# Performance work log

Hardware: AMD Instinct MI355X
Metric: run time of the kernel (lower is better)

The kernel has to match this reference:

```python
import math
import jax, jax.numpy as jnp
import numpy as np

B, N, F, FE = 16, 24, 128, 128   # crystals, atoms/crystal, atom feat, edge feat
NUM_Z = 100                       # num_atomic_numbers
GAUSS_STOP, BASIS_W = 6.0, 1.0
RADIUS_RATE = 1.0
N_CONV, N_FC, FC_F = 3, 4, 128
REP = 1                           # PBC replication per axis (27 images); exact for our cells
ZDIM = 2 * F + FE


def setup_inputs() -> dict:
    key = jax.random.key(0)
    ks = jax.random.split(key, 12)
    # cubic cells with side length in [8, 10) Angstrom -> rep per axis is exactly 1
    L = 8.0 + 2.0 * jax.random.uniform(ks[0], (B,))
    cell = L[:, None, None] * jnp.eye(3, dtype=jnp.float32)          # [B,3,3]
    frac = jax.random.uniform(ks[1], (B, N, 3))
    pos = jnp.einsum('bnd,bde->bne', frac, cell).reshape(B * N, 3)   # [B*N,3]
    atomic_numbers = jax.random.randint(ks[2], (B * N,), 1, NUM_Z + 1)
    batch = jnp.repeat(jnp.arange(B), N)
    emb = jax.random.normal(ks[3], (NUM_Z, F)) * 0.1                 # embedding table
    s = 1.0 / math.sqrt(ZDIM)
    conv_Wf = jax.random.normal(ks[4], (N_CONV, ZDIM, F)) * s
    conv_bf = jnp.zeros((N_CONV, F))
    conv_Ws = jax.random.normal(ks[5], (N_CONV, ZDIM, F)) * s
    conv_bs = jnp.zeros((N_CONV, F))
    sf = 1.0 / math.sqrt(FC_F)
    fc_W = jax.random.normal(ks[6], (N_FC - 1, FC_F, FC_F)) * sf
    fc_b = jnp.zeros((N_FC - 1, FC_F))
    W_out = jax.random.normal(ks[7], (FC_F, 1)) * sf
    b_out = jnp.zeros((1,))
    return {'pos': pos, 'cell': cell, 'emb': emb,
            'conv_Wf': conv_Wf, 'conv_bf': conv_bf,
            'conv_Ws': conv_Ws, 'conv_bs': conv_bs,
            'fc_W': fc_W, 'fc_b': fc_b, 'W_out': W_out, 'b_out': b_out,
            'atomic_numbers': atomic_numbers, 'batch': batch}


def _spectral_normalize(W, iters=5, eps=1e-12):
    # power iteration; sigma differentiable through W only (u,v detached) as in torch
    u = jnp.ones((W.shape[1],), W.dtype)
    u = u / jnp.linalg.norm(u)
    for _ in range(iters):
        v = W @ u
        v = v / (jnp.linalg.norm(v) + eps)
        u = W.T @ v
        u = u / (jnp.linalg.norm(u) + eps)
    u = jax.lax.stop_gradient(u)
    v = jax.lax.stop_gradient(v)
    sigma = v @ (W @ u)
    return W / sigma


def _forward(pos, cell, emb, conv_Wf, conv_bf, conv_Ws, conv_bs,
             fc_W, fc_b, W_out, b_out, atomic_numbers):
    # ---- graph construction (PBC all-pairs, fixed 27 images, masked) ----
    r = jnp.arange(-REP, REP + 1, dtype=cell.dtype)
    grid = jnp.stack(jnp.meshgrid(r, r, r, indexing='ij'), -1).reshape(-1, 3)  # [27,3]
    pbc = jnp.einsum('cd,bde->bce', grid, cell)                                # [B,27,3]
    posb = pos.reshape(B, N, 3)
    # disp[b,i,j,c] = pos_i - (pos_j + offset_c)
    disp = posb[:, :, None, None, :] - (posb[:, None, :, None, :] + pbc[:, None, None, :, :])
    dsqr = jnp.sum(disp * disp, -1)                                            # [B,N,N,27]
    cross = jnp.cross(cell[:, 1], cell[:, 2])
    vol = jnp.sum(cell[:, 0] * cross, -1)
    radius = RADIUS_RATE * (jnp.abs(vol) / N) ** (1.0 / 3.0)                   # [B]
    rb = radius[:, None, None, None]
    mask = (dsqr <= rb * rb) & (dsqr > 1e-4)
    dist = jnp.sqrt(jnp.maximum(dsqr, 1e-12))
    mf = mask.astype(pos.dtype)
    edge_w = (jnp.cos(dist * math.pi / rb) + 1.0) * mf                         # [B,N,N,27]
    # GaussianSmearing
    goff = jnp.linspace(0.0, GAUSS_STOP, FE)
    coeff = -0.5 / (BASIS_W * (goff[1] - goff[0])) ** 2
    edge_attr = jnp.exp(coeff * (dist[..., None] - goff) ** 2)                 # [B,N,N,27,FE]

    # ---- node features ----
    feat = jnp.tanh(emb[atomic_numbers - 1]).reshape(B, N, F)

    # ---- continuous graph convs (CGCNN-style gated conv, edge_weight scaled) ----
    for l in range(N_CONV):
        Wf, Ws = conv_Wf[l], conv_Ws[l]
        gi = feat @ Wf[:F]; gj = feat @ Wf[F:2 * F]
        ge = jnp.einsum('bijce,ef->bijcf', edge_attr, Wf[2 * F:])
        g = jax.nn.sigmoid(gi[:, :, None, None, :] + gj[:, None, :, None, :] + ge + conv_bf[l])
        si = feat @ Ws[:F]; sj = feat @ Ws[F:2 * F]
        se = jnp.einsum('bijce,ef->bijcf', edge_attr, Ws[2 * F:])
        sc = jax.nn.softplus(si[:, :, None, None, :] + sj[:, None, :, None, :] + se + conv_bs[l])
        msg = g * sc * edge_w[..., None]                                       # [B,N,N,27,F]
        feat = jax.nn.softplus(feat + msg.sum((2, 3)))                         # aggregate at i

    # ---- global mean pool + spectral-norm MLP head ----
    h = feat.mean(1)                                                           # [B,F]
    for l in range(N_FC - 1):
        h = jax.nn.softplus(h @ _spectral_normalize(fc_W[l]) + fc_b[l])
    return h @ W_out + b_out                                                   # [B,1]


def reference(pos, cell, emb, conv_Wf, conv_bf, conv_Ws, conv_bs,
              fc_W, fc_b, W_out, b_out, atomic_numbers, batch):
    return _forward(pos, cell, emb, conv_Wf, conv_bf, conv_Ws, conv_bs,
                    fc_W, fc_b, W_out, b_out, atomic_numbers)
```

## Files before the change

kernel.cpp:

```cpp
#include <hip/hip_runtime.h>
#include <math.h>

#define NB 16
#define NN 24
#define NA 384
#define FF 128
#define CC 27
#define MAXNBR 32

__device__ float g_sigma[4];
__device__ float g_projA[NA*4*FF];
__device__ float g_projB[NA*4*FF];
__device__ float g_feat [NA*FF];
__device__ __align__(128) int g_ctr[4*NB][32];
__device__ __align__(128) int g_sigdone[32];
__device__ __align__(128) int g_batchdone[32];

__device__ __forceinline__ float softplusf(float x){ return fmaxf(x,0.f) + log1pf(expf(-fabsf(x))); }
__device__ __forceinline__ float sigmoidf(float x){ return 1.f/(1.f+expf(-x)); }
__device__ __forceinline__ void st_agent(float* p, float v){
  __hip_atomic_store(p, v, __ATOMIC_RELAXED, __HIP_MEMORY_SCOPE_AGENT);
}
__device__ __forceinline__ float ld_agent(const float* p){
  return __hip_atomic_load(p, __ATOMIC_RELAXED, __HIP_MEMORY_SCOPE_AGENT);
}

__device__ __forceinline__ void band_dot(float dist, const float* __restrict__ Wf2,
                                         const float* __restrict__ Ws2, int f,
                                         float& ge, float& se)
{
  const float step  = 6.0f/127.0f;
  const float coeff = -0.5f/(step*step);
  int kmin = (int)ceilf(dist/step - 9.0f);
  kmin = kmin < 0 ? 0 : (kmin > 108 ? 108 : kmin);
  float g = 0.f, s = 0.f;
  #pragma unroll
  for (int t = 0; t < 20; t++) {
    int k = kmin + t;
    float dd = dist - step*(float)k;
    float a  = expf(coeff*dd*dd);
    g += a * Wf2[k*FF+f];
    s += a * Ws2[k*FF+f];
  }
  ge = g; se = s;
}

__device__ __forceinline__ float gemv_q(const float* __restrict__ Wf,
                                        const float* __restrict__ Ws,
                                        const float* s_ft, int q, int f)
{
  const float* W = (q==0) ? Wf : (q==1) ? (Wf + FF*FF) : (q==2) ? Ws : (Ws + FF*FF);
  float s = 0.f;
  #pragma unroll 16
  for (int k = 0; k < FF; k++) s += s_ft[k]*W[k*FF+f];
  return s;
}

__device__ __forceinline__ void publish(int* ctr)
{
  asm volatile("s_waitcnt vmcnt(0)" ::: "memory");
  __syncthreads();
  if (threadIdx.x == 0)
    __hip_atomic_fetch_add(ctr, 1, __ATOMIC_RELAXED, __HIP_MEMORY_SCOPE_AGENT);
}

__device__ __forceinline__ void wait_ge(int* ctr, int target)
{
  if (threadIdx.x == 0) {
    int guard = 0;
    while (__hip_atomic_load(ctr, __ATOMIC_RELAXED, __HIP_MEMORY_SCOPE_AGENT) < target) {
      __builtin_amdgcn_s_sleep(4);
      if (++guard > (1<<18)) break;
    }
  }
  __syncthreads();
}

__device__ __forceinline__ void edge_layer(int l, int q, int f, int n, int i,
       const float* __restrict__ projSrc,
       const float* __restrict__ conv_Wf, const float* __restrict__ conv_bf,
       const float* __restrict__ conv_Ws, const float* __restrict__ conv_bs,
       const int* s_nj, const float* s_nd, const float* s_nw,
       float (*s_p)[FF], float (*sm)[FF], float* s_ft)
{
  const float* Wf2 = conv_Wf + l*3*FF*FF + 2*FF*FF;
  const float* Ws2 = conv_Ws + l*3*FF*FF + 2*FF*FF;
  const float gi  = s_p[0][f];
  const float si  = s_p[2][f];
  const float bff = conv_bf[l*FF+f];
  const float bsf = conv_bs[l*FF+f];
  float msg = 0.f;
  for (int e = q; e < n; e += 4) {
    const int   jg   = s_nj[e];
    const float dist = s_nd[e];
    const float w    = s_nw[e];
    const float gj   = ld_agent(&projSrc[(jg*4+1)*FF+f]);
    const float sj   = ld_agent(&projSrc[(jg*4+3)*FF+f]);
    float ge, se;
    band_dot(dist, Wf2, Ws2, f, ge, se);
    msg += sigmoidf(gi + gj + ge + bff) * softplusf(si + sj + se + bsf) * w;
  }
  sm[q][f] = msg;
  __syncthreads();
  if (threadIdx.x < FF) {
    float v = softplusf(s_ft[f] + sm[0][f] + sm[1][f] + sm[2][f] + sm[3][f]);
    s_ft[f] = v;
  }
  __syncthreads();
}

__global__ void __launch_bounds__(512, 4)
k_fused(const float* __restrict__ pos, const float* __restrict__ cell,
        const float* __restrict__ emb,
        const float* __restrict__ conv_Wf, const float* __restrict__ conv_bf,
        const float* __restrict__ conv_Ws, const float* __restrict__ conv_bs,
        const float* __restrict__ fc_W,  const float* __restrict__ fc_b,
        const float* __restrict__ W_out, const float* __restrict__ b_out,
        const int* __restrict__ z, float* __restrict__ out)
{
  const int tid = threadIdx.x;
  const int q = tid >> 7, f = tid & 127;

  if (blockIdx.x < 3) {
    const int m = blockIdx.x;
    const float* W = fc_W + m*FF*FF;
    __shared__ float s_u[FF], s_v[FF], s_red2[FF];
    __shared__ float s_part2[4][FF];
    if (tid < FF) s_u[tid] = 0.08838834764831845f;
    __syncthreads();
    for (int it = 0; it < 5; it++) {
      { float p = 0.f;
        #pragma unroll
        for (int k = q*32; k < q*32+32; k++) p += W[f*FF+k]*s_u[k];
        s_part2[q][f] = p; }
      __syncthreads();
      if (tid < FF) { float s = s_part2[0][f]+s_part2[1][f]+s_part2[2][f]+s_part2[3][f];
                      s_v[f] = s; s_red2[f] = s*s; }
      __syncthreads();
      for (int st=64; st>0; st>>=1){ if (tid<st) s_red2[tid]+=s_red2[tid+st]; __syncthreads(); }
      float nv = sqrtf(s_red2[0]) + 1e-12f;
      __syncthreads();
      if (tid < FF) s_v[f] /= nv;
      __syncthreads();
      { float p = 0.f;
        #pragma unroll
        for (int r = q*32; r < q*32+32; r++) p += W[r*FF+f]*s_v[r];
        s_part2[q][f] = p; }
      __syncthreads();
      if (tid < FF) { float s = s_part2[0][f]+s_part2[1][f]+s_part2[2][f]+s_part2[3][f];
                      s_u[f] = s; s_red2[f] = s*s; }
      __syncthreads();
      for (int st=64; st>0; st>>=1){ if (tid<st) s_red2[tid]+=s_red2[tid+st]; __syncthreads(); }
      float nu = sqrtf(s_red2[0]) + 1e-12f;
      __syncthreads();
      if (tid < FF) s_u[f] /= nu;
      __syncthreads();
    }
    { float p = 0.f;
      #pragma unroll
      for (int k = q*32; k < q*32+32; k++) p += W[f*FF+k]*s_u[k];
      s_part2[q][f] = p; }
    __syncthreads();
    if (tid < FF) s_red2[f] = s_v[f]*(s_part2[0][f]+s_part2[1][f]+s_part2[2][f]+s_part2[3][f]);
    __syncthreads();
    for (int st=64; st>0; st>>=1){ if (tid<st) s_red2[tid]+=s_red2[tid+st]; __syncthreads(); }
    if (tid == 0) {
      st_agent(&g_sigma[m], s_red2[0]);
      asm volatile("s_waitcnt vmcnt(0)" ::: "memory");
      __hip_atomic_fetch_add(&g_sigdone[0], 1, __ATOMIC_RELAXED, __HIP_MEMORY_SCOPE_AGENT);
    }
    return;
  }

  const int i = (int)blockIdx.x - 3;
  const int b = i / NN;

  __shared__ float s_ft[FF];
  __shared__ float s_cell[9];
  __shared__ float s_rb;
  __shared__ int   s_cnt;
  __shared__ int   s_nj[MAXNBR];
  __shared__ float s_nd[MAXNBR];
  __shared__ float s_nw[MAXNBR];
  __shared__ float s_p[4][FF];
  __shared__ float sm[4][FF];
  __shared__ int   s_last;
  __shared__ float s_hh[FF], s_tmp[FF], s_red[FF];

  if (tid < FF) {
    int zi = z[i]; if (zi < 1) zi = 1; if (zi > 100) zi = 100;
    s_ft[tid] = tanhf(emb[(zi-1)*FF+tid]);
  }
  if (tid >= 256 && tid < 265) s_cell[tid-256] = cell[b*9 + tid - 256];
  if (tid == 500) s_cnt = 0;
  __syncthreads();
  if (tid == 0) {
    const float* c = s_cell;
    float cx = c[4]*c[8] - c[5]*c[7];
    float cy = c[5]*c[6] - c[3]*c[8];
    float cz = c[3]*c[7] - c[4]*c[6];
    float vol = c[0]*cx + c[1]*cy + c[2]*cz;
    s_rb = cbrtf(fabsf(vol)/(float)NN);
  }
  __syncthreads();
  {
    const float rb = s_rb, rb2 = rb*rb;
    const float pix = pos[i*3+0], piy = pos[i*3+1], piz = pos[i*3+2];
    const float PI = 3.14159265358979323846f;
    for (int cand = tid; cand < NN*CC; cand += 512) {
      int j = cand / CC, c = cand - j*CC;
      float gx = (float)(c/9) - 1.0f;
      float gy = (float)((c/3)%3) - 1.0f;
      float gz = (float)(c%3) - 1.0f;
      float ox = gx*s_cell[0] + gy*s_cell[3] + gz*s_cell[6];
      float oy = gx*s_cell[1] + gy*s_cell[4] + gz*s_cell[7];
      float oz = gx*s_cell[2] + gy*s_cell[5] + gz*s_cell[8];
      int jg = b*NN + j;
      float dx = pix - (pos[jg*3+0] + ox);
      float dy = piy - (pos[jg*3+1] + oy);
      float dz = piz - (pos[jg*3+2] + oz);
      float d2 = dx*dx + dy*dy + dz*dz;
      if (d2 <= rb2 && d2 > 1e-4f) {
        float dist = sqrtf(fmaxf(d2, 1e-4f));
        float w = cosf(dist*PI/rb) + 1.0f;
        int slot = atomicAdd(&s_cnt, 1);
        if (slot < MAXNBR) { s_nj[slot] = jg; s_nd[slot] = dist; s_nw[slot] = w; }
      }
    }
  }
  __syncthreads();
  const int n = (s_cnt > MAXNBR) ? MAXNBR : s_cnt;

  { float s0 = gemv_q(conv_Wf, conv_Ws, s_ft, q, f);
    s_p[q][f] = s0;
    st_agent(&g_projA[(i*4+q)*FF+f], s0); }
  publish(&g_ctr[0*NB+b][0]);
  wait_ge(&g_ctr[0*NB+b][0], NN);

  edge_layer(0, q, f, n, i, g_projA, conv_Wf, conv_bf, conv_Ws, conv_bs,
             s_nj, s_nd, s_nw, s_p, sm, s_ft);
  { float s1 = gemv_q(conv_Wf + 3*FF*FF, conv_Ws + 3*FF*FF, s_ft, q, f);
    s_p[q][f] = s1;
    st_agent(&g_projB[(i*4+q)*FF+f], s1); }
  publish(&g_ctr[1*NB+b][0]);
  wait_ge(&g_ctr[1*NB+b][0], NN);

  edge_layer(1, q, f, n, i, g_projB, conv_Wf, conv_bf, conv_Ws, conv_bs,
             s_nj, s_nd, s_nw, s_p, sm, s_ft);
  { float s2 = gemv_q(conv_Wf + 2*3*FF*FF, conv_Ws + 2*3*FF*FF, s_ft, q, f);
    s_p[q][f] = s2;
    st_agent(&g_projA[(i*4+q)*FF+f], s2); }
  publish(&g_ctr[2*NB+b][0]);
  wait_ge(&g_ctr[2*NB+b][0], NN);

  edge_layer(2, q, f, n, i, g_projA, conv_Wf, conv_bf, conv_Ws, conv_bs,
             s_nj, s_nd, s_nw, s_p, sm, s_ft);
  if (tid < FF) st_agent(&g_feat[i*FF+f], s_ft[f]);
  asm volatile("s_waitcnt vmcnt(0)" ::: "memory");
  __syncthreads();
  if (tid == 0)
    s_last = __hip_atomic_fetch_add(&g_ctr[3*NB+b][0], 1, __ATOMIC_RELAXED,
                                    __HIP_MEMORY_SCOPE_AGENT);
  __syncthreads();
  if (s_last != NN-1) return;

  if (tid == 0) {
    int guard = 0;
    while (__hip_atomic_load(&g_sigdone[0], __ATOMIC_RELAXED, __HIP_MEMORY_SCOPE_AGENT) < 3) {
      __builtin_amdgcn_s_sleep(4);
      if (++guard > (1<<18)) break;
    }
  }
  __syncthreads();
  if (tid < FF) {
    float s0 = 0.f;
    for (int a = 0; a < NN; a++) s0 += ld_agent(&g_feat[(b*NN+a)*FF+tid]);
    s_hh[tid] = s0/(float)NN;
  }
  __syncthreads();
  for (int l = 0; l < 3; l++) {
    { float p = 0.f;
      #pragma unroll
      for (int k = q*32; k < q*32+32; k++) p += s_hh[k]*fc_W[l*FF*FF + k*FF + f];
      sm[q][f] = p; }
    __syncthreads();
    if (tid < FF) {
      float s = sm[0][tid]+sm[1][tid]+sm[2][tid]+sm[3][tid];
      s_tmp[tid] = softplusf(s/ld_agent(&g_sigma[l]) + fc_b[l*FF+tid]);
    }
    __syncthreads();
    if (tid < FF) s_hh[tid] = s_tmp[tid];
    __syncthreads();
  }
  if (tid < FF) s_red[tid] = s_hh[tid]*W_out[tid];
  __syncthreads();
  if (tid < 64) {
    float t = s_red[tid] + s_red[tid+64];
    #pragma unroll
    for (int off = 32; off > 0; off >>= 1) t += __shfl_xor(t, off);
    if (tid == 0) {
      out[b] = t + b_out[0];
      __hip_atomic_store(&g_ctr[0*NB+b][0], 0, __ATOMIC_RELAXED, __HIP_MEMORY_SCOPE_AGENT);
      __hip_atomic_store(&g_ctr[1*NB+b][0], 0, __ATOMIC_RELAXED, __HIP_MEMORY_SCOPE_AGENT);
      __hip_atomic_store(&g_ctr[2*NB+b][0], 0, __ATOMIC_RELAXED, __HIP_MEMORY_SCOPE_AGENT);
      __hip_atomic_store(&g_ctr[3*NB+b][0], 0, __ATOMIC_RELAXED, __HIP_MEMORY_SCOPE_AGENT);
      int d = __hip_atomic_fetch_add(&g_batchdone[0], 1, __ATOMIC_RELAXED,
                                     __HIP_MEMORY_SCOPE_AGENT);
      if (d == NB-1) {
        __hip_atomic_store(&g_batchdone[0], 0, __ATOMIC_RELAXED, __HIP_MEMORY_SCOPE_AGENT);
        __hip_atomic_store(&g_sigdone[0],   0, __ATOMIC_RELAXED, __HIP_MEMORY_SCOPE_AGENT);
      }
    }
  }
}

extern "C" void kernel_launch(void* const* d_in, const int* in_sizes, int n_in,
                              void* d_out, int out_size, void* d_ws, size_t ws_size,
                              hipStream_t stream) {
  const float* pos     = (const float*)d_in[0];
  const float* cell    = (const float*)d_in[1];
  const float* emb     = (const float*)d_in[2];
  const float* conv_Wf = (const float*)d_in[3];
  const float* conv_bf = (const float*)d_in[4];
  const float* conv_Ws = (const float*)d_in[5];
  const float* conv_bs = (const float*)d_in[6];
  const float* fc_W    = (const float*)d_in[7];
  const float* fc_b    = (const float*)d_in[8];
  const float* W_out   = (const float*)d_in[9];
  const float* b_out   = (const float*)d_in[10];
  const int*   z       = (const int*)d_in[11];

  k_fused<<<NA+3, 512, 0, stream>>>(pos, cell, emb, conv_Wf, conv_bf,
                                    conv_Ws, conv_bs, fc_W, fc_b,
                                    W_out, b_out, z, (float*)d_out);
}
```

Baseline: 146.4 us.

## Process each crystal in one 1024-thread block with shared-memory projections

Replaces the per-atom grid of 384 blocks with one block per crystal. All 24 atoms' features, projections and neighbor lists now live in shared memory, which removes the global-memory projection buffers and the spin-wait counters between layers. The mean pool no longer needs a last-block election, and the pairwise neighbor search for the whole crystal runs inside the block. In exchange only 19 blocks occupy the GPU, so each block carries far more serial work per thread. The per-atom neighbor cap also drops from 32 to 24.

```diff
diff --git a/kernel.cpp b/kernel.cpp
--- a/kernel.cpp
+++ b/kernel.cpp
@@ -3,16 +3,12 @@
 
 #define NB 16
 #define NN 24
-#define NA 384
 #define FF 128
 #define CC 27
-#define MAXNBR 32
+#define MAXN 24
+#define NCAND (NN*NN*CC)
 
 __device__ float g_sigma[4];
-__device__ float g_projA[NA*4*FF];
-__device__ float g_projB[NA*4*FF];
-__device__ float g_feat [NA*FF];
-__device__ __align__(128) int g_ctr[4*NB][32];
 __device__ __align__(128) int g_sigdone[32];
 __device__ __align__(128) int g_batchdone[32];
 
@@ -45,71 +41,7 @@
   ge = g; se = s;
 }
 
-__device__ __forceinline__ float gemv_q(const float* __restrict__ Wf,
-                                        const float* __restrict__ Ws,
-                                        const float* s_ft, int q, int f)
-{
-  const float* W = (q==0) ? Wf : (q==1) ? (Wf + FF*FF) : (q==2) ? Ws : (Ws + FF*FF);
-  float s = 0.f;
-  #pragma unroll 16
-  for (int k = 0; k < FF; k++) s += s_ft[k]*W[k*FF+f];
-  return s;
-}
-
-__device__ __forceinline__ void publish(int* ctr)
-{
-  asm volatile("s_waitcnt vmcnt(0)" ::: "memory");
-  __syncthreads();
-  if (threadIdx.x == 0)
-    __hip_atomic_fetch_add(ctr, 1, __ATOMIC_RELAXED, __HIP_MEMORY_SCOPE_AGENT);
-}
-
-__device__ __forceinline__ void wait_ge(int* ctr, int target)
-{
-  if (threadIdx.x == 0) {
-    int guard = 0;
-    while (__hip_atomic_load(ctr, __ATOMIC_RELAXED, __HIP_MEMORY_SCOPE_AGENT) < target) {
-      __builtin_amdgcn_s_sleep(4);
-      if (++guard > (1<<18)) break;
-    }
-  }
-  __syncthreads();
-}
-
-__device__ __forceinline__ void edge_layer(int l, int q, int f, int n, int i,
-       const float* __restrict__ projSrc,
-       const float* __restrict__ conv_Wf, const float* __restrict__ conv_bf,
-       const float* __restrict__ conv_Ws, const float* __restrict__ conv_bs,
-       const int* s_nj, const float* s_nd, const float* s_nw,
-       float (*s_p)[FF], float (*sm)[FF], float* s_ft)
-{
-  const float* Wf2 = conv_Wf + l*3*FF*FF + 2*FF*FF;
-  const float* Ws2 = conv_Ws + l*3*FF*FF + 2*FF*FF;
-  const float gi  = s_p[0][f];
-  const float si  = s_p[2][f];
-  const float bff = conv_bf[l*FF+f];
-  const float bsf = conv_bs[l*FF+f];
-  float msg = 0.f;
-  for (int e = q; e < n; e += 4) {
-    const int   jg   = s_nj[e];
-    const float dist = s_nd[e];
-    const float w    = s_nw[e];
-    const float gj   = ld_agent(&projSrc[(jg*4+1)*FF+f]);
-    const float sj   = ld_agent(&projSrc[(jg*4+3)*FF+f]);
-    float ge, se;
-    band_dot(dist, Wf2, Ws2, f, ge, se);
-    msg += sigmoidf(gi + gj + ge + bff) * softplusf(si + sj + se + bsf) * w;
-  }
-  sm[q][f] = msg;
-  __syncthreads();
-  if (threadIdx.x < FF) {
-    float v = softplusf(s_ft[f] + sm[0][f] + sm[1][f] + sm[2][f] + sm[3][f]);
-    s_ft[f] = v;
-  }
-  __syncthreads();
-}
-
-__global__ void __launch_bounds__(512, 4)
+__global__ void __launch_bounds__(1024, 4)
 k_fused(const float* __restrict__ pos, const float* __restrict__ cell,
         const float* __restrict__ emb,
         const float* __restrict__ conv_Wf, const float* __restrict__ conv_bf,
@@ -119,80 +51,82 @@
         const int* __restrict__ z, float* __restrict__ out)
 {
   const int tid = threadIdx.x;
-  const int q = tid >> 7, f = tid & 127;
-
-  if (blockIdx.x < 3) {
-    const int m = blockIdx.x;
+
+  __shared__ float s_ft[NN*FF];
+  __shared__ float s_pj[NN*2*FF];
+  __shared__ float s_part2[4][FF];
+  __shared__ float s_hh[FF], s_tmp[FF], s_red[FF];
+  __shared__ float s_u[FF], s_v[FF];
+  __shared__ float s_pos[NN*3];
+  __shared__ float s_cell[9];
+  __shared__ float s_rb;
+  __shared__ int   s_cnt[NN];
+  __shared__ int   s_nbrj[NN*MAXN];
+  __shared__ float s_nbrd[NN*MAXN];
+  __shared__ float s_nbrw[NN*MAXN];
+
+  if (blockIdx.x >= NB) {
+    const int m = blockIdx.x - NB;
+    const int q = tid >> 7, f = tid & 127;
     const float* W = fc_W + m*FF*FF;
-    __shared__ float s_u[FF], s_v[FF], s_red2[FF];
-    __shared__ float s_part2[4][FF];
     if (tid < FF) s_u[tid] = 0.08838834764831845f;
     __syncthreads();
     for (int it = 0; it < 5; it++) {
-      { float p = 0.f;
+      if (tid < 512) { float p = 0.f;
         #pragma unroll
         for (int k = q*32; k < q*32+32; k++) p += W[f*FF+k]*s_u[k];
         s_part2[q][f] = p; }
       __syncthreads();
       if (tid < FF) { float s = s_part2[0][f]+s_part2[1][f]+s_part2[2][f]+s_part2[3][f];
-                      s_v[f] = s; s_red2[f] = s*s; }
-      __syncthreads();
-      for (int st=64; st>0; st>>=1){ if (tid<st) s_red2[tid]+=s_red2[tid+st]; __syncthreads(); }
-      float nv = sqrtf(s_red2[0]) + 1e-12f;
+                      s_v[f] = s; s_red[f] = s*s; }
+      __syncthreads();
+      for (int st=64; st>0; st>>=1){ if (tid<st) s_red[tid]+=s_red[tid+st]; __syncthreads(); }
+      float nv = sqrtf(s_red[0]) + 1e-12f;
       __syncthreads();
       if (tid < FF) s_v[f] /= nv;
       __syncthreads();
-      { float p = 0.f;
+      if (tid < 512) { float p = 0.f;
         #pragma unroll
         for (int r = q*32; r < q*32+32; r++) p += W[r*FF+f]*s_v[r];
         s_part2[q][f] = p; }
       __syncthreads();
       if (tid < FF) { float s = s_part2[0][f]+s_part2[1][f]+s_part2[2][f]+s_part2[3][f];
-                      s_u[f] = s; s_red2[f] = s*s; }
-      __syncthreads();
-      for (int st=64; st>0; st>>=1){ if (tid<st) s_red2[tid]+=s_red2[tid+st]; __syncthreads(); }
-      float nu = sqrtf(s_red2[0]) + 1e-12f;
+                      s_u[f] = s; s_red[f] = s*s; }
+      __syncthreads();
+      for (int st=64; st>0; st>>=1){ if (tid<st) s_red[tid]+=s_red[tid+st]; __syncthreads(); }
+      float nu = sqrtf(s_red[0]) + 1e-12f;
       __syncthreads();
       if (tid < FF) s_u[f] /= nu;
       __syncthreads();
     }
-    { float p = 0.f;
+    if (tid < 512) { float p = 0.f;
       #pragma unroll
       for (int k = q*32; k < q*32+32; k++) p += W[f*FF+k]*s_u[k];
       s_part2[q][f] = p; }
     __syncthreads();
-    if (tid < FF) s_red2[f] = s_v[f]*(s_part2[0][f]+s_part2[1][f]+s_part2[2][f]+s_part2[3][f]);
-    __syncthreads();
-    for (int st=64; st>0; st>>=1){ if (tid<st) s_red2[tid]+=s_red2[tid+st]; __syncthreads(); }
+    if (tid < FF) s_red[f] = s_v[f]*(s_part2[0][f]+s_part2[1][f]+s_part2[2][f]+s_part2[3][f]);
+    __syncthreads();
+    for (int st=64; st>0; st>>=1){ if (tid<st) s_red[tid]+=s_red[tid+st]; __syncthreads(); }
     if (tid == 0) {
-      st_agent(&g_sigma[m], s_red2[0]);
+      st_agent(&g_sigma[m], s_red[0]);
       asm volatile("s_waitcnt vmcnt(0)" ::: "memory");
       __hip_atomic_fetch_add(&g_sigdone[0], 1, __ATOMIC_RELAXED, __HIP_MEMORY_SCOPE_AGENT);
     }
     return;
   }
 
-  const int i = (int)blockIdx.x - 3;
-  const int b = i / NN;
-
-  __shared__ float s_ft[FF];
-  __shared__ float s_cell[9];
-  __shared__ float s_rb;
-  __shared__ int   s_cnt;
-  __shared__ int   s_nj[MAXNBR];
-  __shared__ float s_nd[MAXNBR];
-  __shared__ float s_nw[MAXNBR];
-  __shared__ float s_p[4][FF];
-  __shared__ float sm[4][FF];
-  __shared__ int   s_last;
-  __shared__ float s_hh[FF], s_tmp[FF], s_red[FF];
-
-  if (tid < FF) {
-    int zi = z[i]; if (zi < 1) zi = 1; if (zi > 100) zi = 100;
-    s_ft[tid] = tanhf(emb[(zi-1)*FF+tid]);
-  }
-  if (tid >= 256 && tid < 265) s_cell[tid-256] = cell[b*9 + tid - 256];
-  if (tid == 500) s_cnt = 0;
+  const int b = blockIdx.x;
+
+  if (tid < 9)    s_cell[tid] = cell[b*9 + tid];
+  if (tid < NN)   s_cnt[tid] = 0;
+  if (tid < NN*3) s_pos[tid] = pos[b*NN*3 + tid];
+  #pragma unroll
+  for (int it = 0; it < 3; ++it) {
+    int idx = tid + it*1024;
+    int i = idx >> 7;
+    int zi = z[b*NN + i]; if (zi < 1) zi = 1; if (zi > 100) zi = 100;
+    s_ft[idx] = tanhf(emb[(zi-1)*FF + (idx & 127)]);
+  }
   __syncthreads();
   if (tid == 0) {
     const float* c = s_cell;
@@ -203,66 +137,113 @@
     s_rb = cbrtf(fabsf(vol)/(float)NN);
   }
   __syncthreads();
+
   {
     const float rb = s_rb, rb2 = rb*rb;
-    const float pix = pos[i*3+0], piy = pos[i*3+1], piz = pos[i*3+2];
     const float PI = 3.14159265358979323846f;
-    for (int cand = tid; cand < NN*CC; cand += 512) {
-      int j = cand / CC, c = cand - j*CC;
-      float gx = (float)(c/9) - 1.0f;
-      float gy = (float)((c/3)%3) - 1.0f;
-      float gz = (float)(c%3) - 1.0f;
-      float ox = gx*s_cell[0] + gy*s_cell[3] + gz*s_cell[6];
-      float oy = gx*s_cell[1] + gy*s_cell[4] + gz*s_cell[7];
-      float oz = gx*s_cell[2] + gy*s_cell[5] + gz*s_cell[8];
-      int jg = b*NN + j;
-      float dx = pix - (pos[jg*3+0] + ox);
-      float dy = piy - (pos[jg*3+1] + oy);
-      float dz = piz - (pos[jg*3+2] + oz);
-      float d2 = dx*dx + dy*dy + dz*dz;
-      if (d2 <= rb2 && d2 > 1e-4f) {
-        float dist = sqrtf(fmaxf(d2, 1e-4f));
-        float w = cosf(dist*PI/rb) + 1.0f;
-        int slot = atomicAdd(&s_cnt, 1);
-        if (slot < MAXNBR) { s_nj[slot] = jg; s_nd[slot] = dist; s_nw[slot] = w; }
+    #pragma unroll
+    for (int it = 0; it < 16; ++it) {
+      int cand = tid + it*1024;
+      if (cand < NCAND) {
+        int i  = cand / (NN*CC);
+        int rem = cand - i*(NN*CC);
+        int j  = rem / CC;
+        int c  = rem - j*CC;
+        float gx = (float)(c/9) - 1.0f;
+        float gy = (float)((c/3)%3) - 1.0f;
+        float gz = (float)(c%3) - 1.0f;
+        float ox = gx*s_cell[0] + gy*s_cell[3] + gz*s_cell[6];
+        float oy = gx*s_cell[1] + gy*s_cell[4] + gz*s_cell[7];
+        float oz = gx*s_cell[2] + gy*s_cell[5] + gz*s_cell[8];
+        float dx = s_pos[i*3+0] - (s_pos[j*3+0] + ox);
+        float dy = s_pos[i*3+1] - (s_pos[j*3+1] + oy);
+        float dz = s_pos[i*3+2] - (s_pos[j*3+2] + oz);
+        float d2 = dx*dx + dy*dy + dz*dz;
+        if (d2 <= rb2 && d2 > 1e-4f) {
+          float dist = sqrtf(fmaxf(d2, 1e-4f));
+          float w = cosf(dist*PI/rb) + 1.0f;
+          int slot = atomicAdd(&s_cnt[i], 1);
+          if (slot < MAXN) {
+            s_nbrj[i*MAXN+slot] = j;
+            s_nbrd[i*MAXN+slot] = dist;
+            s_nbrw[i*MAXN+slot] = w;
+          }
+        }
       }
     }
   }
   __syncthreads();
-  const int n = (s_cnt > MAXNBR) ? MAXNBR : s_cnt;
-
-  { float s0 = gemv_q(conv_Wf, conv_Ws, s_ft, q, f);
-    s_p[q][f] = s0;
-    st_agent(&g_projA[(i*4+q)*FF+f], s0); }
-  publish(&g_ctr[0*NB+b][0]);
-  wait_ge(&g_ctr[0*NB+b][0], NN);
-
-  edge_layer(0, q, f, n, i, g_projA, conv_Wf, conv_bf, conv_Ws, conv_bs,
-             s_nj, s_nd, s_nw, s_p, sm, s_ft);
-  { float s1 = gemv_q(conv_Wf + 3*FF*FF, conv_Ws + 3*FF*FF, s_ft, q, f);
-    s_p[q][f] = s1;
-    st_agent(&g_projB[(i*4+q)*FF+f], s1); }
-  publish(&g_ctr[1*NB+b][0]);
-  wait_ge(&g_ctr[1*NB+b][0], NN);
-
-  edge_layer(1, q, f, n, i, g_projB, conv_Wf, conv_bf, conv_Ws, conv_bs,
-             s_nj, s_nd, s_nw, s_p, sm, s_ft);
-  { float s2 = gemv_q(conv_Wf + 2*3*FF*FF, conv_Ws + 2*3*FF*FF, s_ft, q, f);
-    s_p[q][f] = s2;
-    st_agent(&g_projA[(i*4+q)*FF+f], s2); }
-  publish(&g_ctr[2*NB+b][0]);
-  wait_ge(&g_ctr[2*NB+b][0], NN);
-
-  edge_layer(2, q, f, n, i, g_projA, conv_Wf, conv_bf, conv_Ws, conv_bs,
-             s_nj, s_nd, s_nw, s_p, sm, s_ft);
-  if (tid < FF) st_agent(&g_feat[i*FF+f], s_ft[f]);
-  asm volatile("s_waitcnt vmcnt(0)" ::: "memory");
-  __syncthreads();
-  if (tid == 0)
-    s_last = __hip_atomic_fetch_add(&g_ctr[3*NB+b][0], 1, __ATOMIC_RELAXED,
-                                    __HIP_MEMORY_SCOPE_AGENT);
-  __syncthreads();
-  if (s_last != NN-1) return;
+
+  float pregi[3], presi[3];
+
+  #define PROJ_PASS(WfL, WsL, rowoff)                                     \
+  { _Pragma("unroll")                                                     \
+    for (int it2 = 0; it2 < 6; ++it2) {                                   \
+      int idx = tid + it2*1024;                                           \
+      int i = idx >> 8, h = (idx >> 7) & 1, f = idx & 127;                \
+      const float* W = ((h==0) ? (WfL) : (WsL)) + (rowoff);               \
+      float s = 0.f;                                                      \
+      _Pragma("unroll 16")                                                \
+      for (int k = 0; k < FF; ++k) s += s_ft[i*FF+k]*W[k*FF+f];           \
+      s_pj[(i*2+h)*FF+f] = s;                                             \
+    } }
+
+  #define READ_OWN()                                                      \
+  { _Pragma("unroll")                                                     \
+    for (int it2 = 0; it2 < 3; ++it2) {                                   \
+      int idx = tid + it2*1024;                                           \
+      int i = idx >> 7, f = idx & 127;                                    \
+      pregi[it2] = s_pj[(i*2+0)*FF+f];                                    \
+      presi[it2] = s_pj[(i*2+1)*FF+f];                                    \
+    } }
+
+  PROJ_PASS(conv_Wf, conv_Ws, 0);
+  __syncthreads();
+  READ_OWN();
+  __syncthreads();
+  PROJ_PASS(conv_Wf, conv_Ws, FF*FF);
+  __syncthreads();
+
+  #define EDGE_TERM(e, acc)                                               \
+  { int j = s_nbrj[i*MAXN+(e)];                                           \
+    float dist = s_nbrd[i*MAXN+(e)];                                      \
+    float w    = s_nbrw[i*MAXN+(e)];                                      \
+    float gj = s_pj[(j*2+0)*FF+f];                                        \
+    float sj = s_pj[(j*2+1)*FF+f];                                        \
+    float ge, se; band_dot(dist, Wf2, Ws2, f, ge, se);                    \
+    acc += sigmoidf(gi + gj + ge + bff) * softplusf(si + sj + se + bsf) * w; }
+
+  for (int l = 0; l < 3; ++l) {
+    const float* Wf2 = conv_Wf + l*3*FF*FF + 2*FF*FF;
+    const float* Ws2 = conv_Ws + l*3*FF*FF + 2*FF*FF;
+    #pragma unroll
+    for (int it2 = 0; it2 < 3; ++it2) {
+      int idx = tid + it2*1024;
+      int i = idx >> 7, f = idx & 127;
+      const float gi = pregi[it2], si = presi[it2];
+      const float bff = conv_bf[l*FF+f], bsf = conv_bs[l*FF+f];
+      int n = s_cnt[i]; if (n > MAXN) n = MAXN;
+      float m0=0.f, m1=0.f, m2=0.f, m3=0.f;
+      for (int e = 0; e < n; e += 4) {
+        EDGE_TERM(e, m0);
+        if (e+1 < n) EDGE_TERM(e+1, m1);
+        if (e+2 < n) EDGE_TERM(e+2, m2);
+        if (e+3 < n) EDGE_TERM(e+3, m3);
+      }
+      s_ft[idx] = softplusf(s_ft[idx] + m0 + m1 + m2 + m3);
+    }
+    __syncthreads();
+    if (l < 2) {
+      const float* Wfn = conv_Wf + (l+1)*3*FF*FF;
+      const float* Wsn = conv_Ws + (l+1)*3*FF*FF;
+      PROJ_PASS(Wfn, Wsn, 0);
+      __syncthreads();
+      READ_OWN();
+      __syncthreads();
+      PROJ_PASS(Wfn, Wsn, FF*FF);
+      __syncthreads();
+    }
+  }
 
   if (tid == 0) {
     int guard = 0;
@@ -274,18 +255,21 @@
   __syncthreads();
   if (tid < FF) {
     float s0 = 0.f;
-    for (int a = 0; a < NN; a++) s0 += ld_agent(&g_feat[(b*NN+a)*FF+tid]);
+    for (int a = 0; a < NN; ++a) s0 += s_ft[a*FF+tid];
     s_hh[tid] = s0/(float)NN;
   }
   __syncthreads();
-  for (int l = 0; l < 3; l++) {
-    { float p = 0.f;
+  for (int l = 0; l < 3; ++l) {
+    if (tid < 512) {
+      const int q = tid >> 7, f = tid & 127;
+      float p = 0.f;
       #pragma unroll
-      for (int k = q*32; k < q*32+32; k++) p += s_hh[k]*fc_W[l*FF*FF + k*FF + f];
-      sm[q][f] = p; }
+      for (int k = q*32; k < q*32+32; ++k) p += s_hh[k]*fc_W[l*FF*FF + k*FF + f];
+      s_part2[q][f] = p;
+    }
     __syncthreads();
     if (tid < FF) {
-      float s = sm[0][tid]+sm[1][tid]+sm[2][tid]+sm[3][tid];
+      float s = s_part2[0][tid]+s_part2[1][tid]+s_part2[2][tid]+s_part2[3][tid];
       s_tmp[tid] = softplusf(s/ld_agent(&g_sigma[l]) + fc_b[l*FF+tid]);
     }
     __syncthreads();
@@ -300,10 +284,6 @@
     for (int off = 32; off > 0; off >>= 1) t += __shfl_xor(t, off);
     if (tid == 0) {
       out[b] = t + b_out[0];
-      __hip_atomic_store(&g_ctr[0*NB+b][0], 0, __ATOMIC_RELAXED, __HIP_MEMORY_SCOPE_AGENT);
-      __hip_atomic_store(&g_ctr[1*NB+b][0], 0, __ATOMIC_RELAXED, __HIP_MEMORY_SCOPE_AGENT);
-      __hip_atomic_store(&g_ctr[2*NB+b][0], 0, __ATOMIC_RELAXED, __HIP_MEMORY_SCOPE_AGENT);
-      __hip_atomic_store(&g_ctr[3*NB+b][0], 0, __ATOMIC_RELAXED, __HIP_MEMORY_SCOPE_AGENT);
       int d = __hip_atomic_fetch_add(&g_batchdone[0], 1, __ATOMIC_RELAXED,
                                      __HIP_MEMORY_SCOPE_AGENT);
       if (d == NB-1) {
@@ -330,7 +310,7 @@
   const float* b_out   = (const float*)d_in[10];
   const int*   z       = (const int*)d_in[11];
 
-  k_fused<<<NA+3, 512, 0, stream>>>(pos, cell, emb, conv_Wf, conv_bf,
-                                    conv_Ws, conv_bs, fc_W, fc_b,
-                                    W_out, b_out, z, (float*)d_out);
-}
+  k_fused<<<NB+3, 1024, 0, stream>>>(pos, cell, emb, conv_Wf, conv_bf,
+                                     conv_Ws, conv_bs, fc_W, fc_b,
+                                     W_out, b_out, z, (float*)d_out);
+}
```

Result: slower. 454.5 us (+210.5%).

## Process two atoms per block and precompute Gaussian basis values in shared memory

Applied to the files above, without the earlier changes.

Each block now handles two atoms instead of one, which halves the grid and lets both atoms share weight loads in the projection GEMVs and edge band dots. The per-crystal barrier counters now wait for 12 blocks instead of 24. Gaussian expansion values and band offsets are computed once per edge into shared memory and reused across all three conv layers, so the band dot no longer recomputes expf for every feature thread. Spin-wait sleep intervals are shortened. In exchange each block does more serial work and uses more shared memory, and the grid is half as large.

```diff
diff --git a/kernel.cpp b/kernel.cpp
--- a/kernel.cpp
+++ b/kernel.cpp
@@ -7,6 +7,8 @@
 #define FF 128
 #define CC 27
 #define MAXNBR 32
+#define BPB 12
+#define NT 20
 
 __device__ float g_sigma[4];
 __device__ float g_projA[NA*4*FF];
@@ -25,20 +27,16 @@
   return __hip_atomic_load(p, __ATOMIC_RELAXED, __HIP_MEMORY_SCOPE_AGENT);
 }
 
-__device__ __forceinline__ void band_dot(float dist, const float* __restrict__ Wf2,
-                                         const float* __restrict__ Ws2, int f,
-                                         float& ge, float& se)
-{
-  const float step  = 6.0f/127.0f;
-  const float coeff = -0.5f/(step*step);
-  int kmin = (int)ceilf(dist/step - 9.0f);
-  kmin = kmin < 0 ? 0 : (kmin > 108 ? 108 : kmin);
+__device__ __forceinline__ void band_dot2(const float* __restrict__ ga, int kmin,
+                                          const float* __restrict__ Wf2,
+                                          const float* __restrict__ Ws2, int f,
+                                          float& ge, float& se)
+{
   float g = 0.f, s = 0.f;
   #pragma unroll
-  for (int t = 0; t < 20; t++) {
+  for (int t = 0; t < NT; t++) {
+    float a = ga[t];
     int k = kmin + t;
-    float dd = dist - step*(float)k;
-    float a  = expf(coeff*dd*dd);
     g += a * Wf2[k*FF+f];
     s += a * Ws2[k*FF+f];
   }
@@ -69,42 +67,9 @@
   if (threadIdx.x == 0) {
     int guard = 0;
     while (__hip_atomic_load(ctr, __ATOMIC_RELAXED, __HIP_MEMORY_SCOPE_AGENT) < target) {
-      __builtin_amdgcn_s_sleep(4);
-      if (++guard > (1<<18)) break;
-    }
-  }
-  __syncthreads();
-}
-
-__device__ __forceinline__ void edge_layer(int l, int q, int f, int n, int i,
-       const float* __restrict__ projSrc,
-       const float* __restrict__ conv_Wf, const float* __restrict__ conv_bf,
-       const float* __restrict__ conv_Ws, const float* __restrict__ conv_bs,
-       const int* s_nj, const float* s_nd, const float* s_nw,
-       float (*s_p)[FF], float (*sm)[FF], float* s_ft)
-{
-  const float* Wf2 = conv_Wf + l*3*FF*FF + 2*FF*FF;
-  const float* Ws2 = conv_Ws + l*3*FF*FF + 2*FF*FF;
-  const float gi  = s_p[0][f];
-  const float si  = s_p[2][f];
-  const float bff = conv_bf[l*FF+f];
-  const float bsf = conv_bs[l*FF+f];
-  float msg = 0.f;
-  for (int e = q; e < n; e += 4) {
-    const int   jg   = s_nj[e];
-    const float dist = s_nd[e];
-    const float w    = s_nw[e];
-    const float gj   = ld_agent(&projSrc[(jg*4+1)*FF+f]);
-    const float sj   = ld_agent(&projSrc[(jg*4+3)*FF+f]);
-    float ge, se;
-    band_dot(dist, Wf2, Ws2, f, ge, se);
-    msg += sigmoidf(gi + gj + ge + bff) * softplusf(si + sj + se + bsf) * w;
-  }
-  sm[q][f] = msg;
-  __syncthreads();
-  if (threadIdx.x < FF) {
-    float v = softplusf(s_ft[f] + sm[0][f] + sm[1][f] + sm[2][f] + sm[3][f]);
-    s_ft[f] = v;
+      __builtin_amdgcn_s_sleep(2);
+      if (++guard > (1<<19)) break;
+    }
   }
   __syncthreads();
 }
@@ -172,27 +137,31 @@
     return;
   }
 
-  const int i = (int)blockIdx.x - 3;
-  const int b = i / NN;
-
-  __shared__ float s_ft[FF];
+  const int p_  = (int)blockIdx.x - 3;
+  const int i0  = 2*p_;
+  const int b   = i0 / NN;
+
+  __shared__ float s_ft[2][FF];
   __shared__ float s_cell[9];
   __shared__ float s_rb;
-  __shared__ int   s_cnt;
-  __shared__ int   s_nj[MAXNBR];
-  __shared__ float s_nd[MAXNBR];
-  __shared__ float s_nw[MAXNBR];
-  __shared__ float s_p[4][FF];
-  __shared__ float sm[4][FF];
+  __shared__ int   s_cnt[2];
+  __shared__ int   s_nj[2][MAXNBR];
+  __shared__ float s_nd[2][MAXNBR];
+  __shared__ float s_nw[2][MAXNBR];
+  __shared__ float s_ga[2][MAXNBR][NT];
+  __shared__ int   s_km[2][MAXNBR];
+  __shared__ float s_p[2][4][FF];
+  __shared__ float sm[2][4][FF];
   __shared__ int   s_last;
   __shared__ float s_hh[FF], s_tmp[FF], s_red[FF];
 
-  if (tid < FF) {
-    int zi = z[i]; if (zi < 1) zi = 1; if (zi > 100) zi = 100;
-    s_ft[tid] = tanhf(emb[(zi-1)*FF+tid]);
+  if (tid < 2*FF) {
+    int a = tid >> 7, ff = tid & 127;
+    int zi = z[i0 + a]; if (zi < 1) zi = 1; if (zi > 100) zi = 100;
+    s_ft[a][ff] = tanhf(emb[(zi-1)*FF+ff]);
   }
   if (tid >= 256 && tid < 265) s_cell[tid-256] = cell[b*9 + tid - 256];
-  if (tid == 500) s_cnt = 0;
+  if (tid == 500) { s_cnt[0] = 0; s_cnt[1] = 0; }
   __syncthreads();
   if (tid == 0) {
     const float* c = s_cell;
@@ -203,72 +172,126 @@
     s_rb = cbrtf(fabsf(vol)/(float)NN);
   }
   __syncthreads();
+
   {
     const float rb = s_rb, rb2 = rb*rb;
-    const float pix = pos[i*3+0], piy = pos[i*3+1], piz = pos[i*3+2];
     const float PI = 3.14159265358979323846f;
-    for (int cand = tid; cand < NN*CC; cand += 512) {
-      int j = cand / CC, c = cand - j*CC;
-      float gx = (float)(c/9) - 1.0f;
-      float gy = (float)((c/3)%3) - 1.0f;
-      float gz = (float)(c%3) - 1.0f;
-      float ox = gx*s_cell[0] + gy*s_cell[3] + gz*s_cell[6];
-      float oy = gx*s_cell[1] + gy*s_cell[4] + gz*s_cell[7];
-      float oz = gx*s_cell[2] + gy*s_cell[5] + gz*s_cell[8];
-      int jg = b*NN + j;
-      float dx = pix - (pos[jg*3+0] + ox);
-      float dy = piy - (pos[jg*3+1] + oy);
-      float dz = piz - (pos[jg*3+2] + oz);
-      float d2 = dx*dx + dy*dy + dz*dz;
-      if (d2 <= rb2 && d2 > 1e-4f) {
-        float dist = sqrtf(fmaxf(d2, 1e-4f));
-        float w = cosf(dist*PI/rb) + 1.0f;
-        int slot = atomicAdd(&s_cnt, 1);
-        if (slot < MAXNBR) { s_nj[slot] = jg; s_nd[slot] = dist; s_nw[slot] = w; }
+    for (int a = 0; a < 2; ++a) {
+      const int i = i0 + a;
+      const float pix = pos[i*3+0], piy = pos[i*3+1], piz = pos[i*3+2];
+      for (int cand = tid; cand < NN*CC; cand += 512) {
+        int j = cand / CC, c = cand - j*CC;
+        float gx = (float)(c/9) - 1.0f;
+        float gy = (float)((c/3)%3) - 1.0f;
+        float gz = (float)(c%3) - 1.0f;
+        float ox = gx*s_cell[0] + gy*s_cell[3] + gz*s_cell[6];
+        float oy = gx*s_cell[1] + gy*s_cell[4] + gz*s_cell[7];
+        float oz = gx*s_cell[2] + gy*s_cell[5] + gz*s_cell[8];
+        int jg = b*NN + j;
+        float dx = pix - (pos[jg*3+0] + ox);
+        float dy = piy - (pos[jg*3+1] + oy);
+        float dz = piz - (pos[jg*3+2] + oz);
+        float d2 = dx*dx + dy*dy + dz*dz;
+        if (d2 <= rb2 && d2 > 1e-4f) {
+          float dist = sqrtf(fmaxf(d2, 1e-4f));
+          float w = cosf(dist*PI/rb) + 1.0f;
+          int slot = atomicAdd(&s_cnt[a], 1);
+          if (slot < MAXNBR) { s_nj[a][slot] = jg; s_nd[a][slot] = dist; s_nw[a][slot] = w; }
+        }
       }
     }
   }
   __syncthreads();
-  const int n = (s_cnt > MAXNBR) ? MAXNBR : s_cnt;
-
-  { float s0 = gemv_q(conv_Wf, conv_Ws, s_ft, q, f);
-    s_p[q][f] = s0;
-    st_agent(&g_projA[(i*4+q)*FF+f], s0); }
+
+  for (int idx = tid; idx < 2*MAXNBR*NT; idx += 512) {
+    int a = idx / (MAXNBR*NT);
+    int r = idx - a*(MAXNBR*NT);
+    int e = r / NT, t = r - e*NT;
+    int n = s_cnt[a]; if (n > MAXNBR) n = MAXNBR;
+    if (e < n) {
+      float dist = s_nd[a][e];
+      const float step  = 6.0f/127.0f;
+      const float coeff = -0.5f/(step*step);
+      int kmin = (int)ceilf(dist/step - 9.0f);
+      kmin = kmin < 0 ? 0 : (kmin > 108 ? 108 : kmin);
+      if (t == 0) s_km[a][e] = kmin;
+      int k = kmin + t;
+      float dd = dist - step*(float)k;
+      s_ga[a][e][t] = expf(coeff*dd*dd);
+    }
+  }
+  __syncthreads();
+
+  #pragma unroll
+  for (int a = 0; a < 2; ++a) {
+    float s0 = gemv_q(conv_Wf, conv_Ws, s_ft[a], q, f);
+    s_p[a][q][f] = s0;
+    st_agent(&g_projA[((i0+a)*4+q)*FF+f], s0);
+  }
   publish(&g_ctr[0*NB+b][0]);
-  wait_ge(&g_ctr[0*NB+b][0], NN);
-
-  edge_layer(0, q, f, n, i, g_projA, conv_Wf, conv_bf, conv_Ws, conv_bs,
-             s_nj, s_nd, s_nw, s_p, sm, s_ft);
-  { float s1 = gemv_q(conv_Wf + 3*FF*FF, conv_Ws + 3*FF*FF, s_ft, q, f);
-    s_p[q][f] = s1;
-    st_agent(&g_projB[(i*4+q)*FF+f], s1); }
-  publish(&g_ctr[1*NB+b][0]);
-  wait_ge(&g_ctr[1*NB+b][0], NN);
-
-  edge_layer(1, q, f, n, i, g_projB, conv_Wf, conv_bf, conv_Ws, conv_bs,
-             s_nj, s_nd, s_nw, s_p, sm, s_ft);
-  { float s2 = gemv_q(conv_Wf + 2*3*FF*FF, conv_Ws + 2*3*FF*FF, s_ft, q, f);
-    s_p[q][f] = s2;
-    st_agent(&g_projA[(i*4+q)*FF+f], s2); }
-  publish(&g_ctr[2*NB+b][0]);
-  wait_ge(&g_ctr[2*NB+b][0], NN);
-
-  edge_layer(2, q, f, n, i, g_projA, conv_Wf, conv_bf, conv_Ws, conv_bs,
-             s_nj, s_nd, s_nw, s_p, sm, s_ft);
-  if (tid < FF) st_agent(&g_feat[i*FF+f], s_ft[f]);
+  wait_ge(&g_ctr[0*NB+b][0], BPB);
+
+  for (int l = 0; l < 3; ++l) {
+    const float* projSrc = (l==1) ? g_projB : g_projA;
+    const float* Wf2 = conv_Wf + l*3*FF*FF + 2*FF*FF;
+    const float* Ws2 = conv_Ws + l*3*FF*FF + 2*FF*FF;
+    const float bff = conv_bf[l*FF+f];
+    const float bsf = conv_bs[l*FF+f];
+    #pragma unroll
+    for (int a = 0; a < 2; ++a) {
+      const float gi = s_p[a][0][f], si = s_p[a][2][f];
+      int n = s_cnt[a]; if (n > MAXNBR) n = MAXNBR;
+      float msg = 0.f;
+      for (int e = q; e < n; e += 4) {
+        int   jg   = s_nj[a][e];
+        float w    = s_nw[a][e];
+        float gj = ld_agent(&projSrc[(jg*4+1)*FF+f]);
+        float sj = ld_agent(&projSrc[(jg*4+3)*FF+f]);
+        float ge, se;
+        band_dot2(&s_ga[a][e][0], s_km[a][e], Wf2, Ws2, f, ge, se);
+        msg += sigmoidf(gi + gj + ge + bff) * softplusf(si + sj + se + bsf) * w;
+      }
+      sm[a][q][f] = msg;
+    }
+    __syncthreads();
+    if (tid < 2*FF) {
+      int a = tid >> 7, ff = tid & 127;
+      s_ft[a][ff] = softplusf(s_ft[a][ff] + sm[a][0][ff] + sm[a][1][ff]
+                                          + sm[a][2][ff] + sm[a][3][ff]);
+    }
+    __syncthreads();
+    if (l < 2) {
+      const float* WfN = conv_Wf + (l+1)*3*FF*FF;
+      const float* WsN = conv_Ws + (l+1)*3*FF*FF;
+      float* projDst = (l==0) ? g_projB : g_projA;
+      #pragma unroll
+      for (int a = 0; a < 2; ++a) {
+        float s1 = gemv_q(WfN, WsN, s_ft[a], q, f);
+        s_p[a][q][f] = s1;
+        st_agent(&projDst[((i0+a)*4+q)*FF+f], s1);
+      }
+      publish(&g_ctr[(l+1)*NB+b][0]);
+      wait_ge(&g_ctr[(l+1)*NB+b][0], BPB);
+    }
+  }
+
+  if (tid < 2*FF) {
+    int a = tid >> 7, ff = tid & 127;
+    st_agent(&g_feat[(i0+a)*FF+ff], s_ft[a][ff]);
+  }
   asm volatile("s_waitcnt vmcnt(0)" ::: "memory");
   __syncthreads();
   if (tid == 0)
     s_last = __hip_atomic_fetch_add(&g_ctr[3*NB+b][0], 1, __ATOMIC_RELAXED,
                                     __HIP_MEMORY_SCOPE_AGENT);
   __syncthreads();
-  if (s_last != NN-1) return;
+  if (s_last != BPB-1) return;
 
   if (tid == 0) {
     int guard = 0;
     while (__hip_atomic_load(&g_sigdone[0], __ATOMIC_RELAXED, __HIP_MEMORY_SCOPE_AGENT) < 3) {
-      __builtin_amdgcn_s_sleep(4);
-      if (++guard > (1<<18)) break;
+      __builtin_amdgcn_s_sleep(2);
+      if (++guard > (1<<19)) break;
     }
   }
   __syncthreads();
@@ -282,10 +305,10 @@
     { float p = 0.f;
       #pragma unroll
       for (int k = q*32; k < q*32+32; k++) p += s_hh[k]*fc_W[l*FF*FF + k*FF + f];
-      sm[q][f] = p; }
+      sm[0][q][f] = p; }
     __syncthreads();
     if (tid < FF) {
-      float s = sm[0][tid]+sm[1][tid]+sm[2][tid]+sm[3][tid];
+      float s = sm[0][0][tid]+sm[0][1][tid]+sm[0][2][tid]+sm[0][3][tid];
       s_tmp[tid] = softplusf(s/ld_agent(&g_sigma[l]) + fc_b[l*FF+tid]);
     }
     __syncthreads();
@@ -330,7 +353,7 @@
   const float* b_out   = (const float*)d_in[10];
   const int*   z       = (const int*)d_in[11];
 
-  k_fused<<<NA+3, 512, 0, stream>>>(pos, cell, emb, conv_Wf, conv_bf,
-                                    conv_Ws, conv_bs, fc_W, fc_b,
-                                    W_out, b_out, z, (float*)d_out);
-}
+  k_fused<<<3 + NA/2, 512, 0, stream>>>(pos, cell, emb, conv_Wf, conv_bf,
+                                        conv_Ws, conv_bs, fc_W, fc_b,
+                                        W_out, b_out, z, (float*)d_out);
+}
```

Result: slower. 169.5 us (+15.8%).
